# Kernel tuning notes

Measured on AMD Instinct MI355X. Metric: run time of the kernel, lower is better.

## Reference

```python
import jax, jax.numpy as jnp
import numpy as np

B_SZ, L_SEQ, D_MODEL, D_STATE = 4, 2048, 1024, 16


def setup_inputs() -> dict:
    key = jax.random.key(0)
    ks = jax.random.split(key, 6)
    x = jax.random.normal(ks[0], (B_SZ, L_SEQ, D_MODEL), jnp.float32)
    # HiPPO-inspired init: A_log = log(arange(1..n)).clamp(min=-7), broadcast over channels
    A_log = jnp.clip(jnp.log(jnp.arange(1, D_STATE + 1, dtype=jnp.float32)), -7.0, None)
    A_log = jnp.broadcast_to(A_log[None, :], (D_MODEL, D_STATE)).astype(jnp.float32)
    B_param = 0.02 * jax.random.normal(ks[1], (D_MODEL, D_STATE), jnp.float32)
    C_param = 0.02 * jax.random.normal(ks[2], (D_MODEL, D_STATE), jnp.float32)
    log_dt = 0.01 * jax.random.normal(ks[3], (D_MODEL,), jnp.float32) - 4.0
    in_w = jax.random.normal(ks[4], (2 * D_MODEL, D_MODEL), jnp.float32) / np.sqrt(D_MODEL).astype(np.float32)
    in_b = jnp.zeros((2 * D_MODEL,), jnp.float32)
    out_w = jax.random.normal(ks[5], (D_MODEL, D_MODEL), jnp.float32) / np.sqrt(D_MODEL).astype(np.float32)
    out_b = jnp.zeros((D_MODEL,), jnp.float32)
    ln_g = jnp.ones((D_MODEL,), jnp.float32)
    ln_b = jnp.zeros((D_MODEL,), jnp.float32)
    return {"x": x, "A_log": A_log, "B_param": B_param, "C_param": C_param,
            "log_dt": log_dt, "in_w": in_w, "in_b": in_b, "out_w": out_w,
            "out_b": out_b, "ln_g": ln_g, "ln_b": ln_b}


def _ssm_scan(u, A_log, B_param, C_param, log_dt):
    # u: (B, L, D). Builds kernel h[t,d] = sum_n A_bar[d,n]^t * C[d,n]*B[d,n]*dt[d]
    # and applies a causal depthwise convolution (via FFT; same math as conv1d).
    L = u.shape[1]
    dt = jnp.clip(jnp.exp(log_dt), 1e-4, 1.0)                      # (D,)
    A_bar = jnp.exp(-jnp.exp(A_log) * dt[:, None])                 # ZOH discretisation (D,N)
    A_bar = jnp.clip(A_bar, 1e-8, 1.0 - 1e-8)
    log_A = jnp.log(A_bar)                                         # (D,N)
    t_idx = jnp.arange(L, dtype=jnp.float32)                       # (L,)
    A_powers = jnp.exp(t_idx[:, None, None] * log_A[None, :, :])   # (L,D,N)
    cb_dt = C_param * B_param * dt[:, None]                        # (D,N)
    kernel = jnp.einsum('ldn,dn->ld', A_powers, cb_dt)             # (L,D)
    # causal conv: y[b,t,d] = sum_{tau<=t} kernel[tau,d] * u[b,t-tau,d]
    n_fft = 2 * L
    Kf = jnp.fft.rfft(kernel, n=n_fft, axis=0)                     # (n_fft/2+1, D)
    Uf = jnp.fft.rfft(u, n=n_fft, axis=1)                          # (B, n_fft/2+1, D)
    y = jnp.fft.irfft(Uf * Kf[None], n=n_fft, axis=1)[:, :L]       # (B,L,D)
    return y.astype(u.dtype)


def reference(x, A_log, B_param, C_param, log_dt, in_w, in_b, out_w, out_b, ln_g, ln_b):
    x = x.astype(jnp.float32)
    residual = x
    # LayerNorm (eps=1e-5)
    mu = jnp.mean(x, axis=-1, keepdims=True)
    var = jnp.mean(jnp.square(x - mu), axis=-1, keepdims=True)
    xn = (x - mu) * jax.lax.rsqrt(var + 1e-5) * ln_g + ln_b
    xz = xn @ in_w.T + in_b                                        # (B,L,2D)
    x_proj, z = xz[..., :D_MODEL], xz[..., D_MODEL:]
    z = jax.nn.silu(z)
    y = _ssm_scan(x_proj, A_log, B_param, C_param, log_dt)
    y = y * z
    y = y @ out_w.T + out_b
    # dropout is identity in eval mode
    return jnp.clip(y + residual, -10.0, 10.0)
```

## Files before the change

### kernel.cpp

```cpp
#include <hip/hip_runtime.h>
#include <hip/hip_bf16.h>

#define D_MODEL 1024
#define D_STATE 16
#define L_SEQ 2048
#define B_SZ 4
#define M_ROWS (B_SZ * L_SEQ)
#define N_CHUNK 32
#define C_LEN 64

typedef __attribute__((ext_vector_type(8))) short short8;
typedef __attribute__((ext_vector_type(4))) float f32x4;

#define SBAR()  asm volatile("s_barrier" ::: "memory")
#define GATE(N) asm volatile("s_waitcnt vmcnt(" #N ") lgkmcnt(0)\n\ts_barrier" ::: "memory")

typedef const unsigned short __attribute__((address_space(1))) gas_us;
typedef unsigned short __attribute__((address_space(3))) las_us;
static __device__ __forceinline__ void gload16(const unsigned short* g, unsigned short* l) {
    __builtin_amdgcn_global_load_lds((gas_us*)g, (las_us*)l, 16, 0, 0);
}

static __device__ __forceinline__ unsigned short f2bf(float f) {
    unsigned int u = __float_as_uint(f);
    unsigned int r = (u + 0x7FFFu + ((u >> 16) & 1u)) >> 16;
    return (unsigned short)r;
}
static __device__ __forceinline__ float bf2f(unsigned short u) {
    return __uint_as_float(((unsigned int)u) << 16);
}

__global__ __launch_bounds__(256) void prep_kernel(const float* __restrict__ x,
                                                   const float* __restrict__ g,
                                                   const float* __restrict__ b,
                                                   unsigned short* __restrict__ xn,
                                                   const float* __restrict__ in_w,
                                                   unsigned short* __restrict__ w1,
                                                   const float* __restrict__ out_w,
                                                   unsigned short* __restrict__ w2) {
    __shared__ float sbuf[8];
    int bid = blockIdx.x;
    int t = threadIdx.x;
    if (bid < M_ROWS) {
        int row = bid;
        const float4* xr = (const float4*)(x + (size_t)row * D_MODEL);
        float4 v = xr[t];
        float s  = v.x + v.y + v.z + v.w;
        float ss = v.x * v.x + v.y * v.y + v.z * v.z + v.w * v.w;
        #pragma unroll
        for (int o = 32; o > 0; o >>= 1) {
            s  += __shfl_down(s,  o);
            ss += __shfl_down(ss, o);
        }
        int wid = t >> 6;
        if ((t & 63) == 0) { sbuf[wid] = s; sbuf[4 + wid] = ss; }
        __syncthreads();
        float S  = sbuf[0] + sbuf[1] + sbuf[2] + sbuf[3];
        float SS = sbuf[4] + sbuf[5] + sbuf[6] + sbuf[7];
        float mu  = S * (1.0f / D_MODEL);
        float var = SS * (1.0f / D_MODEL) - mu * mu;
        float inv = rsqrtf(var + 1e-5f);
        float4 gv = ((const float4*)g)[t];
        float4 bv = ((const float4*)b)[t];
        ushort4 o;
        o.x = f2bf((v.x - mu) * inv * gv.x + bv.x);
        o.y = f2bf((v.y - mu) * inv * gv.y + bv.y);
        o.z = f2bf((v.z - mu) * inv * gv.z + bv.z);
        o.w = f2bf((v.w - mu) * inv * gv.w + bv.w);
        ((ushort4*)(xn + (size_t)row * D_MODEL))[t] = o;
    } else if (bid < M_ROWS + 2048) {
        int i = (bid - M_ROWS) * 256 + t;
        float4 v = ((const float4*)in_w)[i];
        ushort4 o;
        o.x = f2bf(v.x); o.y = f2bf(v.y); o.z = f2bf(v.z); o.w = f2bf(v.w);
        ((ushort4*)w1)[i] = o;
    } else {
        int i = (bid - M_ROWS - 2048) * 256 + t;
        float4 v = ((const float4*)out_w)[i];
        ushort4 o;
        o.x = f2bf(v.x); o.y = f2bf(v.y); o.z = f2bf(v.z); o.w = f2bf(v.w);
        ((ushort4*)w2)[i] = o;
    }
}

#define MFMA32(ACC, AV, BV) { \
    _Pragma("unroll") for (int i_ = 0; i_ < 8; ++i_) { \
        _Pragma("unroll") for (int jf_ = 0; jf_ < 4; ++jf_) \
            ACC[i_][jf_] = __builtin_amdgcn_mfma_f32_16x16x32_bf16( \
                AV[i_], BV[jf_], ACC[i_][jf_], 0, 0, 0); } }

#define STAGE1(J) { size_t ko_ = (size_t)(J) * 32; int so_ = ((J) & 3) * 16384; \
    gload16(pA0 + ko_, dA0 + so_); gload16(pA1 + ko_, dA1 + so_); \
    gload16(pB0 + ko_, dB0 + so_); gload16(pB1 + ko_, dB1 + so_); }

#define G1_TILE(J, DOSTAGE, TRAIL) { \
    const int slot_ = (J) & 3; \
    const char* rA_ = ldsA_rd + slot_ * 32768; \
    const char* rB_ = ldsB_rd + slot_ * 32768; \
    short8 av[8], bv[4]; \
    _Pragma("unroll") for (int i_ = 0; i_ < 8; ++i_) av[i_] = *(const short8*)(rA_ + i_ * 1024); \
    _Pragma("unroll") for (int j_ = 0; j_ < 4; ++j_) bv[j_] = *(const short8*)(rB_ + j_ * 1024); \
    if (DOSTAGE) { STAGE1((J) + 3); } \
    SBAR(); \
    __builtin_amdgcn_s_setprio(1); \
    MFMA32(acc, av, bv); \
    __builtin_amdgcn_s_setprio(0); \
    TRAIL; \
}

__global__ __launch_bounds__(512, 1) void gemm1_kernel(const unsigned short* __restrict__ A,
                                                       const unsigned short* __restrict__ Bt,
                                                       const float* __restrict__ bias,
                                                       unsigned short* __restrict__ u_bf,
                                                       unsigned short* __restrict__ zs) {
    __shared__ __align__(16) unsigned short lds[4][16384];
    const int K = D_MODEL;

    int t = threadIdx.x;
    int lane = t & 63;
    int wave = t >> 6;
    int wm = wave >> 2;
    int wn = wave & 3;

    int bid = blockIdx.x;
    int swz = (bid & 7) * 32 + (bid >> 3);
    int m0 = (swz >> 3) * 256;
    int n0 = (swz & 7) * 256;

    int srow = lane >> 2;
    int sk = ((lane & 3) * 8) ^ ((lane & 32) >> 1);
    const unsigned short* pA0 = A  + (size_t)(m0 + wave * 16 + srow) * K + sk;
    const unsigned short* pA1 = pA0 + (size_t)128 * K;
    const unsigned short* pB0 = Bt + (size_t)(n0 + wave * 16 + srow) * K + sk;
    const unsigned short* pB1 = pB0 + (size_t)128 * K;

    unsigned short* dA0 = &lds[0][wave * 512];
    unsigned short* dA1 = &lds[0][4096 + wave * 512];
    unsigned short* dB0 = &lds[0][8192 + wave * 512];
    unsigned short* dB1 = &lds[0][12288 + wave * 512];

    int off_base = (lane & 15) * 64 + (((lane >> 4) * 16) ^ ((lane & 8) * 4));
    const char* ldsA_rd = (const char*)(&lds[0][0]) + wm * 8192 + off_base;
    const char* ldsB_rd = (const char*)(&lds[0][0]) + 16384 + wn * 4096 + off_base;

    f32x4 acc[8][4] = {};

    STAGE1(0); STAGE1(1); STAGE1(2);
    GATE(8);

    #pragma unroll 1
    for (int j = 0; j < 29; ++j) { G1_TILE(j, true, GATE(8)); }
    G1_TILE(29, false, GATE(4));
    G1_TILE(30, false, GATE(0));
    G1_TILE(31, false, (void)0);

    int col = lane & 15;
    int quad = lane >> 4;
    float bs[4];
    #pragma unroll
    for (int jf = 0; jf < 4; ++jf) bs[jf] = bias[n0 + wn * 64 + jf * 16 + col];
    bool isU = (n0 < D_MODEL);
    int nbase = isU ? (n0 + wn * 64 + col) : (n0 - D_MODEL + wn * 64 + col);
    unsigned short* obase = isU ? u_bf : zs;
    #pragma unroll
    for (int i = 0; i < 8; ++i) {
        #pragma unroll
        for (int r = 0; r < 4; ++r) {
            int m = m0 + wm * 128 + i * 16 + quad * 4 + r;
            unsigned short* orow = obase + (size_t)m * D_MODEL + nbase;
            #pragma unroll
            for (int jf = 0; jf < 4; ++jf) {
                float v = acc[i][jf][r] + bs[jf];
                if (!isU) v = v / (1.0f + __expf(-v));
                orow[jf * 16] = f2bf(v);
            }
        }
    }
}

#define MFMA16(ACC, AV, BV) { \
    _Pragma("unroll") for (int i_ = 0; i_ < 4; ++i_) { \
        _Pragma("unroll") for (int jf_ = 0; jf_ < 4; ++jf_) \
            ACC[i_][jf_] = __builtin_amdgcn_mfma_f32_16x16x32_bf16( \
                AV[i_], BV[jf_], ACC[i_][jf_], 0, 0, 0); } }

#define STAGE2(J) { size_t ko_ = (size_t)(J) * 32; int so_ = ((J) & 3) * 12288; \
    gload16(pA0 + ko_, dA + so_); gload16(pB0 + ko_, dB0 + so_); gload16(pB1 + ko_, dB1 + so_); }

#define G2_TILE(J, DOSTAGE, TRAIL) { \
    const int slot_ = (J) & 3; \
    const char* rA_ = ldsA_rd + slot_ * 24576; \
    const char* rB_ = ldsB_rd + slot_ * 24576; \
    short8 av[4], bv[4]; \
    _Pragma("unroll") for (int i_ = 0; i_ < 4; ++i_) av[i_] = *(const short8*)(rA_ + i_ * 1024); \
    _Pragma("unroll") for (int j_ = 0; j_ < 4; ++j_) bv[j_] = *(const short8*)(rB_ + j_ * 1024); \
    if (DOSTAGE) { STAGE2((J) + 3); } \
    SBAR(); \
    __builtin_amdgcn_s_setprio(1); \
    MFMA16(acc, av, bv); \
    __builtin_amdgcn_s_setprio(0); \
    TRAIL; \
}

__global__ __launch_bounds__(512, 2) void gemm2_kernel(const unsigned short* __restrict__ A,
                                                       const unsigned short* __restrict__ Bt,
                                                       const float* __restrict__ bias,
                                                       float* __restrict__ out_f,
                                                       const float* __restrict__ resid) {
    __shared__ __align__(16) unsigned short lds[4][12288];
    const int K = D_MODEL;

    int t = threadIdx.x;
    int lane = t & 63;
    int wave = t >> 6;
    int wm = wave >> 2;
    int wn = wave & 3;

    int bid = blockIdx.x;
    int swz = (bid & 7) * 32 + (bid >> 3);
    int m0 = (swz >> 2) * 128;
    int n0 = (swz & 3) * 256;

    int srow = lane >> 2;
    int sk = ((lane & 3) * 8) ^ ((lane & 32) >> 1);
    const unsigned short* pA0 = A  + (size_t)(m0 + wave * 16 + srow) * K + sk;
    const unsigned short* pB0 = Bt + (size_t)(n0 + wave * 16 + srow) * K + sk;
    const unsigned short* pB1 = pB0 + (size_t)128 * K;

    unsigned short* dA  = &lds[0][wave * 512];
    unsigned short* dB0 = &lds[0][4096 + wave * 512];
    unsigned short* dB1 = &lds[0][8192 + wave * 512];

    int off_base = (lane & 15) * 64 + (((lane >> 4) * 16) ^ ((lane & 8) * 4));
    const char* ldsA_rd = (const char*)(&lds[0][0]) + wm * 4096 + off_base;
    const char* ldsB_rd = (const char*)(&lds[0][0]) + 8192 + wn * 4096 + off_base;

    f32x4 acc[4][4] = {};

    STAGE2(0); STAGE2(1); STAGE2(2);
    GATE(6);

    #pragma unroll 1
    for (int j = 0; j < 29; ++j) { G2_TILE(j, true, GATE(6)); }
    G2_TILE(29, false, GATE(3));
    G2_TILE(30, false, GATE(0));
    G2_TILE(31, false, (void)0);

    int col = lane & 15;
    int quad = lane >> 4;
    float bs[4];
    #pragma unroll
    for (int jf = 0; jf < 4; ++jf) bs[jf] = bias[n0 + wn * 64 + jf * 16 + col];
    #pragma unroll
    for (int i = 0; i < 4; ++i) {
        #pragma unroll
        for (int r = 0; r < 4; ++r) {
            int m = m0 + wm * 64 + i * 16 + quad * 4 + r;
            const float* rrow = resid + (size_t)m * D_MODEL + n0 + wn * 64 + col;
            float* orow = out_f + (size_t)m * D_MODEL + n0 + wn * 64 + col;
            #pragma unroll
            for (int jf = 0; jf < 4; ++jf) {
                float y = acc[i][jf][r] + bs[jf] + rrow[jf * 16];
                y = fminf(10.0f, fmaxf(-10.0f, y));
                orow[jf * 16] = y;
            }
        }
    }
}

static __device__ __forceinline__ void load_params(const float* __restrict__ A_log,
                                                   const float* __restrict__ log_dt,
                                                   int d, float* ab, float& dt_out) {
    float dt = fminf(1.0f, fmaxf(1e-4f, __expf(log_dt[d])));
    #pragma unroll
    for (int n = 0; n < D_STATE; n++) {
        float a = __expf(-__expf(A_log[d * D_STATE + n]) * dt);
        ab[n] = fminf(1.0f - 1e-8f, fmaxf(1e-8f, a));
    }
    dt_out = dt;
}

__global__ __launch_bounds__(256) void scan1_kernel(const unsigned short* __restrict__ u,
                                                    const float* __restrict__ A_log,
                                                    const float* __restrict__ log_dt,
                                                    float* __restrict__ s_local) {
    int gid = blockIdx.x * 256 + threadIdx.x;
    int d = gid & (D_MODEL - 1);
    int c = (gid >> 10) & (N_CHUNK - 1);
    int b = gid >> 15;

    float ab[D_STATE], dt;
    load_params(A_log, log_dt, d, ab, dt);

    float s[D_STATE];
    #pragma unroll
    for (int n = 0; n < D_STATE; n++) s[n] = 0.0f;

    const unsigned short* up = u + ((size_t)(b * L_SEQ + c * C_LEN)) * D_MODEL + d;
    for (int t = 0; t < C_LEN; t++) {
        float uv = bf2f(up[(size_t)t * D_MODEL]);
        #pragma unroll
        for (int n = 0; n < D_STATE; n++) s[n] = fmaf(ab[n], s[n], uv);
    }
    float* sl = s_local + ((size_t)(b * N_CHUNK + c) * D_STATE) * D_MODEL + d;
    #pragma unroll
    for (int n = 0; n < D_STATE; n++) sl[(size_t)n * D_MODEL] = s[n];
}

__global__ __launch_bounds__(256) void scan_combine_kernel(const float* __restrict__ s_local,
                                                           const float* __restrict__ A_log,
                                                           const float* __restrict__ log_dt,
                                                           float* __restrict__ s_init) {
    int gid = blockIdx.x * 256 + threadIdx.x;
    int d = gid & (D_MODEL - 1);
    int n = (gid >> 10) & (D_STATE - 1);
    int b = gid >> 14;

    float dt = fminf(1.0f, fmaxf(1e-4f, __expf(log_dt[d])));
    float a = __expf(-__expf(A_log[d * D_STATE + n]) * dt);
    a = fminf(1.0f - 1e-8f, fmaxf(1e-8f, a));
    float aP = a;
    #pragma unroll
    for (int q = 0; q < 6; q++) aP = aP * aP;

    float s = 0.0f;
    size_t stride_c = (size_t)D_STATE * D_MODEL;
    const float* sl = s_local + ((size_t)b * N_CHUNK * D_STATE + n) * D_MODEL + d;
    float* si = s_init + ((size_t)b * N_CHUNK * D_STATE + n) * D_MODEL + d;
    si[0] = 0.0f;
    for (int c = 1; c < N_CHUNK; c++) {
        s = fmaf(aP, s, sl[(size_t)(c - 1) * stride_c]);
        si[(size_t)c * stride_c] = s;
    }
}

__global__ __launch_bounds__(256) void scan2_kernel(const unsigned short* __restrict__ u,
                                                    const unsigned short* __restrict__ zs,
                                                    const float* __restrict__ A_log,
                                                    const float* __restrict__ Bp,
                                                    const float* __restrict__ Cp,
                                                    const float* __restrict__ log_dt,
                                                    const float* __restrict__ s_init,
                                                    unsigned short* __restrict__ yz) {
    int gid = blockIdx.x * 256 + threadIdx.x;
    int d = gid & (D_MODEL - 1);
    int c = (gid >> 10) & (N_CHUNK - 1);
    int b = gid >> 15;

    float ab[D_STATE], dt;
    load_params(A_log, log_dt, d, ab, dt);
    float cb[D_STATE];
    #pragma unroll
    for (int n = 0; n < D_STATE; n++)
        cb[n] = Cp[d * D_STATE + n] * Bp[d * D_STATE + n] * dt;

    float s[D_STATE];
    const float* si = s_init + ((size_t)(b * N_CHUNK + c) * D_STATE) * D_MODEL + d;
    #pragma unroll
    for (int n = 0; n < D_STATE; n++) s[n] = si[(size_t)n * D_MODEL];

    size_t m0 = (size_t)(b * L_SEQ + c * C_LEN);
    const unsigned short* up = u + m0 * D_MODEL + d;
    const unsigned short* zp = zs + m0 * D_MODEL + d;
    unsigned short* yp = yz + m0 * D_MODEL + d;

    for (int t = 0; t < C_LEN; t++) {
        float uv = bf2f(up[(size_t)t * D_MODEL]);
        #pragma unroll
        for (int n = 0; n < D_STATE; n++) s[n] = fmaf(ab[n], s[n], uv);
        float y = 0.0f;
        #pragma unroll
        for (int n = 0; n < D_STATE; n++) y = fmaf(cb[n], s[n], y);
        float zv = bf2f(zp[(size_t)t * D_MODEL]);
        yp[(size_t)t * D_MODEL] = f2bf(y * zv);
    }
}

extern "C" void kernel_launch(void* const* d_in, const int* in_sizes, int n_in,
                              void* d_out, int out_size, void* d_ws, size_t ws_size,
                              hipStream_t stream) {
    const float* x       = (const float*)d_in[0];
    const float* A_log   = (const float*)d_in[1];
    const float* B_param = (const float*)d_in[2];
    const float* C_param = (const float*)d_in[3];
    const float* log_dt  = (const float*)d_in[4];
    const float* in_w    = (const float*)d_in[5];
    const float* in_b    = (const float*)d_in[6];
    const float* out_w   = (const float*)d_in[7];
    const float* out_b   = (const float*)d_in[8];
    const float* ln_g    = (const float*)d_in[9];
    const float* ln_b    = (const float*)d_in[10];
    float* out = (float*)d_out;

    char* ws = (char*)d_ws;
    size_t off = 0;
    unsigned short* xn = (unsigned short*)(ws + off); off += (size_t)M_ROWS * D_MODEL * 2;
    unsigned short* w1 = (unsigned short*)(ws + off); off += (size_t)2 * D_MODEL * D_MODEL * 2;
    unsigned short* u  = (unsigned short*)(ws + off); off += (size_t)M_ROWS * D_MODEL * 2;
    unsigned short* zs = (unsigned short*)(ws + off); off += (size_t)M_ROWS * D_MODEL * 2;
    unsigned short* yz = (unsigned short*)(ws + off); off += (size_t)M_ROWS * D_MODEL * 2;
    unsigned short* w2 = (unsigned short*)(ws + off); off += (size_t)D_MODEL * D_MODEL * 2;
    float* s_local = (float*)(ws + off); off += (size_t)B_SZ * N_CHUNK * D_STATE * D_MODEL * 4;
    float* s_init  = (float*)(ws + off); off += (size_t)B_SZ * N_CHUNK * D_STATE * D_MODEL * 4;

    prep_kernel<<<M_ROWS + 2048 + 1024, 256, 0, stream>>>(x, ln_g, ln_b, xn, in_w, w1, out_w, w2);

    gemm1_kernel<<<256, 512, 0, stream>>>(xn, w1, in_b, u, zs);

    scan1_kernel<<<(B_SZ * N_CHUNK * D_MODEL) / 256, 256, 0, stream>>>(u, A_log, log_dt, s_local);
    scan_combine_kernel<<<(B_SZ * D_STATE * D_MODEL) / 256, 256, 0, stream>>>(s_local, A_log, log_dt, s_init);
    scan2_kernel<<<(B_SZ * N_CHUNK * D_MODEL) / 256, 256, 0, stream>>>(
        u, zs, A_log, B_param, C_param, log_dt, s_init, yz);

    gemm2_kernel<<<256, 512, 0, stream>>>(yz, w2, out_b, out, x);
}
```

Measured before the change: 206.1 us.

## Fuse three-pass chunked scan into one kernel with shared-memory prefix combine

Replaces the scan1, combine and scan2 kernels with one kernel. Each block covers one batch and 16 channels across all 32 chunks, and the chunk states are combined with a log-step prefix scan in shared memory. The u values are cached in registers so u is read once instead of twice, and the s_local/s_init round trips through global memory and two launches go away. In exchange it launches only 256 blocks of 512 threads with heavy register pressure (32 packed u words plus several 16-wide state arrays). Each thread's global accesses now touch 16 contiguous channels (32 bytes) per row instead of full rows, which may hurt coalescing.

```diff
diff --git a/kernel.cpp b/kernel.cpp
--- a/kernel.cpp
+++ b/kernel.cpp
@@ -268,111 +268,111 @@
     }
 }
 
-static __device__ __forceinline__ void load_params(const float* __restrict__ A_log,
-                                                   const float* __restrict__ log_dt,
-                                                   int d, float* ab, float& dt_out) {
+__global__ __launch_bounds__(512) void scan_fused_kernel(const unsigned short* __restrict__ u,
+                                                         const unsigned short* __restrict__ zs,
+                                                         const float* __restrict__ A_log,
+                                                         const float* __restrict__ Bp,
+                                                         const float* __restrict__ Cp,
+                                                         const float* __restrict__ log_dt,
+                                                         unsigned short* __restrict__ yz) {
+    __shared__ float S[N_CHUNK][D_STATE][17];
+
+    int bid = blockIdx.x;
+    int l  = (bid & 7) * 32 + (bid >> 3);
+    int b  = l >> 6;
+    int dg = l & 63;
+    int t  = threadIdx.x;
+    int c  = t >> 4;
+    int dl = t & 15;
+    int d  = dg * 16 + dl;
+
     float dt = fminf(1.0f, fmaxf(1e-4f, __expf(log_dt[d])));
+    float ab[D_STATE];
     #pragma unroll
     for (int n = 0; n < D_STATE; n++) {
         float a = __expf(-__expf(A_log[d * D_STATE + n]) * dt);
         ab[n] = fminf(1.0f - 1e-8f, fmaxf(1e-8f, a));
     }
-    dt_out = dt;
-}
-
-__global__ __launch_bounds__(256) void scan1_kernel(const unsigned short* __restrict__ u,
-                                                    const float* __restrict__ A_log,
-                                                    const float* __restrict__ log_dt,
-                                                    float* __restrict__ s_local) {
-    int gid = blockIdx.x * 256 + threadIdx.x;
-    int d = gid & (D_MODEL - 1);
-    int c = (gid >> 10) & (N_CHUNK - 1);
-    int b = gid >> 15;
-
-    float ab[D_STATE], dt;
-    load_params(A_log, log_dt, d, ab, dt);
-
-    float s[D_STATE];
-    #pragma unroll
-    for (int n = 0; n < D_STATE; n++) s[n] = 0.0f;
-
-    const unsigned short* up = u + ((size_t)(b * L_SEQ + c * C_LEN)) * D_MODEL + d;
-    for (int t = 0; t < C_LEN; t++) {
-        float uv = bf2f(up[(size_t)t * D_MODEL]);
-        #pragma unroll
-        for (int n = 0; n < D_STATE; n++) s[n] = fmaf(ab[n], s[n], uv);
-    }
-    float* sl = s_local + ((size_t)(b * N_CHUNK + c) * D_STATE) * D_MODEL + d;
-    #pragma unroll
-    for (int n = 0; n < D_STATE; n++) sl[(size_t)n * D_MODEL] = s[n];
-}
-
-__global__ __launch_bounds__(256) void scan_combine_kernel(const float* __restrict__ s_local,
-                                                           const float* __restrict__ A_log,
-                                                           const float* __restrict__ log_dt,
-                                                           float* __restrict__ s_init) {
-    int gid = blockIdx.x * 256 + threadIdx.x;
-    int d = gid & (D_MODEL - 1);
-    int n = (gid >> 10) & (D_STATE - 1);
-    int b = gid >> 14;
-
-    float dt = fminf(1.0f, fmaxf(1e-4f, __expf(log_dt[d])));
-    float a = __expf(-__expf(A_log[d * D_STATE + n]) * dt);
-    a = fminf(1.0f - 1e-8f, fmaxf(1e-8f, a));
-    float aP = a;
-    #pragma unroll
-    for (int q = 0; q < 6; q++) aP = aP * aP;
-
-    float s = 0.0f;
-    size_t stride_c = (size_t)D_STATE * D_MODEL;
-    const float* sl = s_local + ((size_t)b * N_CHUNK * D_STATE + n) * D_MODEL + d;
-    float* si = s_init + ((size_t)b * N_CHUNK * D_STATE + n) * D_MODEL + d;
-    si[0] = 0.0f;
-    for (int c = 1; c < N_CHUNK; c++) {
-        s = fmaf(aP, s, sl[(size_t)(c - 1) * stride_c]);
-        si[(size_t)c * stride_c] = s;
-    }
-}
-
-__global__ __launch_bounds__(256) void scan2_kernel(const unsigned short* __restrict__ u,
-                                                    const unsigned short* __restrict__ zs,
-                                                    const float* __restrict__ A_log,
-                                                    const float* __restrict__ Bp,
-                                                    const float* __restrict__ Cp,
-                                                    const float* __restrict__ log_dt,
-                                                    const float* __restrict__ s_init,
-                                                    unsigned short* __restrict__ yz) {
-    int gid = blockIdx.x * 256 + threadIdx.x;
-    int d = gid & (D_MODEL - 1);
-    int c = (gid >> 10) & (N_CHUNK - 1);
-    int b = gid >> 15;
-
-    float ab[D_STATE], dt;
-    load_params(A_log, log_dt, d, ab, dt);
+
+    size_t row0 = (size_t)(b * L_SEQ + c * C_LEN);
+    const unsigned short* up = u + row0 * D_MODEL + d;
+
+    unsigned int uc[32];
+    float P[D_STATE];
+    #pragma unroll
+    for (int n = 0; n < D_STATE; n++) P[n] = 0.0f;
+    #pragma unroll
+    for (int tt = 0; tt < 32; tt++) {
+        unsigned int lo = up[(size_t)(2 * tt) * D_MODEL];
+        unsigned int hi = up[(size_t)(2 * tt + 1) * D_MODEL];
+        uc[tt] = lo | (hi << 16);
+        float u0 = __uint_as_float(lo << 16);
+        float u1 = __uint_as_float(hi << 16);
+        #pragma unroll
+        for (int n = 0; n < D_STATE; n++) P[n] = fmaf(ab[n], P[n], u0);
+        #pragma unroll
+        for (int n = 0; n < D_STATE; n++) P[n] = fmaf(ab[n], P[n], u1);
+    }
+
+    #pragma unroll
+    for (int n = 0; n < D_STATE; n++) S[c][n][dl] = P[n];
+
+    float m[D_STATE];
+    #pragma unroll
+    for (int n = 0; n < D_STATE; n++) {
+        float a2 = ab[n];
+        #pragma unroll
+        for (int q = 0; q < 6; q++) a2 = a2 * a2;
+        m[n] = a2;
+    }
+    __syncthreads();
+
+    #pragma unroll
+    for (int k = 1; k < N_CHUNK; k <<= 1) {
+        float tmp[D_STATE];
+        #pragma unroll
+        for (int n = 0; n < D_STATE; n++) tmp[n] = (c >= k) ? S[c - k][n][dl] : 0.0f;
+        __syncthreads();
+        #pragma unroll
+        for (int n = 0; n < D_STATE; n++) {
+            P[n] = fmaf(m[n], tmp[n], P[n]);
+            S[c][n][dl] = P[n];
+        }
+        #pragma unroll
+        for (int n = 0; n < D_STATE; n++) m[n] = m[n] * m[n];
+        __syncthreads();
+    }
+
+    float s2[D_STATE];
+    #pragma unroll
+    for (int n = 0; n < D_STATE; n++) s2[n] = (c == 0) ? 0.0f : S[c - 1][n][dl];
+
     float cb[D_STATE];
     #pragma unroll
     for (int n = 0; n < D_STATE; n++)
         cb[n] = Cp[d * D_STATE + n] * Bp[d * D_STATE + n] * dt;
 
-    float s[D_STATE];
-    const float* si = s_init + ((size_t)(b * N_CHUNK + c) * D_STATE) * D_MODEL + d;
-    #pragma unroll
-    for (int n = 0; n < D_STATE; n++) s[n] = si[(size_t)n * D_MODEL];
-
-    size_t m0 = (size_t)(b * L_SEQ + c * C_LEN);
-    const unsigned short* up = u + m0 * D_MODEL + d;
-    const unsigned short* zp = zs + m0 * D_MODEL + d;
-    unsigned short* yp = yz + m0 * D_MODEL + d;
-
-    for (int t = 0; t < C_LEN; t++) {
-        float uv = bf2f(up[(size_t)t * D_MODEL]);
-        #pragma unroll
-        for (int n = 0; n < D_STATE; n++) s[n] = fmaf(ab[n], s[n], uv);
-        float y = 0.0f;
-        #pragma unroll
-        for (int n = 0; n < D_STATE; n++) y = fmaf(cb[n], s[n], y);
-        float zv = bf2f(zp[(size_t)t * D_MODEL]);
-        yp[(size_t)t * D_MODEL] = f2bf(y * zv);
+    const unsigned short* zp = zs + row0 * D_MODEL + d;
+    unsigned short* yp = yz + row0 * D_MODEL + d;
+
+    #pragma unroll
+    for (int tt = 0; tt < 32; tt++) {
+        unsigned int w = uc[tt];
+        float u0 = __uint_as_float(w << 16);
+        float u1 = __uint_as_float(w & 0xFFFF0000u);
+        float y0 = 0.0f, y1 = 0.0f;
+        #pragma unroll
+        for (int n = 0; n < D_STATE; n++) s2[n] = fmaf(ab[n], s2[n], u0);
+        #pragma unroll
+        for (int n = 0; n < D_STATE; n++) y0 = fmaf(cb[n], s2[n], y0);
+        #pragma unroll
+        for (int n = 0; n < D_STATE; n++) s2[n] = fmaf(ab[n], s2[n], u1);
+        #pragma unroll
+        for (int n = 0; n < D_STATE; n++) y1 = fmaf(cb[n], s2[n], y1);
+        float z0 = bf2f(zp[(size_t)(2 * tt) * D_MODEL]);
+        float z1 = bf2f(zp[(size_t)(2 * tt + 1) * D_MODEL]);
+        yp[(size_t)(2 * tt) * D_MODEL]     = f2bf(y0 * z0);
+        yp[(size_t)(2 * tt + 1) * D_MODEL] = f2bf(y1 * z1);
     }
 }
 
@@ -400,17 +400,12 @@
     unsigned short* zs = (unsigned short*)(ws + off); off += (size_t)M_ROWS * D_MODEL * 2;
     unsigned short* yz = (unsigned short*)(ws + off); off += (size_t)M_ROWS * D_MODEL * 2;
     unsigned short* w2 = (unsigned short*)(ws + off); off += (size_t)D_MODEL * D_MODEL * 2;
-    float* s_local = (float*)(ws + off); off += (size_t)B_SZ * N_CHUNK * D_STATE * D_MODEL * 4;
-    float* s_init  = (float*)(ws + off); off += (size_t)B_SZ * N_CHUNK * D_STATE * D_MODEL * 4;
 
     prep_kernel<<<M_ROWS + 2048 + 1024, 256, 0, stream>>>(x, ln_g, ln_b, xn, in_w, w1, out_w, w2);
 
     gemm1_kernel<<<256, 512, 0, stream>>>(xn, w1, in_b, u, zs);
 
-    scan1_kernel<<<(B_SZ * N_CHUNK * D_MODEL) / 256, 256, 0, stream>>>(u, A_log, log_dt, s_local);
-    scan_combine_kernel<<<(B_SZ * D_STATE * D_MODEL) / 256, 256, 0, stream>>>(s_local, A_log, log_dt, s_init);
-    scan2_kernel<<<(B_SZ * N_CHUNK * D_MODEL) / 256, 256, 0, stream>>>(
-        u, zs, A_log, B_param, C_param, log_dt, s_init, yz);
+    scan_fused_kernel<<<256, 512, 0, stream>>>(u, zs, A_log, B_param, C_param, log_dt, yz);
 
     gemm2_kernel<<<256, 512, 0, stream>>>(yz, w2, out_b, out, x);
 }
```

Result: faster. 198.1 us (-3.9%).
